# Kernel tuning notes

Hardware: AMD Instinct MI355X
Metric: run time of the kernel (lower is better)

Reference implementation:

```python
import jax, jax.numpy as jnp
import numpy as np

N_NODES = 50000
N_EDGES = 800000
IN_DIM = 128
HID = 128
N_GRAPHS = 64


def setup_inputs() -> dict:
    key = jax.random.key(0)
    ks = jax.random.split(key, 12)
    edge_index = jax.random.randint(ks[0], (2, N_EDGES), 0, N_NODES, dtype=jnp.int64)
    edge_weight = jax.random.uniform(ks[1], (N_EDGES,), dtype=jnp.float32)
    input_feature = jax.random.normal(ks[2], (N_NODES, IN_DIM), dtype=jnp.float32)
    graph_indicator = jnp.sort(jax.random.randint(ks[3], (N_NODES,), 0, N_GRAPHS, dtype=jnp.int64))
    s = 0.05
    W1 = jax.random.normal(ks[4], (IN_DIM, HID), dtype=jnp.float32) * s
    b1 = jnp.zeros((HID,), jnp.float32)
    W2 = jax.random.normal(ks[5], (HID, HID), dtype=jnp.float32) * s
    b2 = jnp.zeros((HID,), jnp.float32)
    W3 = jax.random.normal(ks[6], (HID, HID), dtype=jnp.float32) * s
    b3 = jnp.zeros((HID,), jnp.float32)
    wa = jax.random.normal(ks[7], (3 * HID, 1), dtype=jnp.float32) * s
    ba = jnp.zeros((1,), jnp.float32)
    Wf = jax.random.normal(ks[8], (3 * HID * 2, IN_DIM), dtype=jnp.float32) * s
    bf = jnp.zeros((IN_DIM,), jnp.float32)
    return dict(edge_index=edge_index, edge_weight=edge_weight,
                input_feature=input_feature, graph_indicator=graph_indicator,
                W1=W1, b1=b1, W2=W2, b2=b2, W3=W3, b3=b3,
                wa=wa, ba=ba, Wf=Wf, bf=bf)


def reference(edge_index, edge_weight, input_feature, graph_indicator,
              W1, b1, W2, b2, W3, b3, wa, ba, Wf, bf):
    src, dst = edge_index[0], edge_index[1]

    def gcn(x, W, b):
        # GraphConvolution: adj @ (x @ W) + b, adj given as weighted edge list
        support = x @ W  # [N, d_out]
        msg = edge_weight[:, None] * support[src]  # [E, d_out] gather
        return jax.ops.segment_sum(msg, dst, num_segments=N_NODES) + b

    g1 = jax.nn.relu(gcn(input_feature, W1, b1))
    g2 = jax.nn.relu(gcn(g1, W2, b2))
    g3 = jax.nn.relu(gcn(g2, W3, b3))
    h = jnp.concatenate([g1, g2, g3], axis=1)  # [N, 3*HID]

    # SelfAttentionPooling: attention score via a 1-dim GraphConvolution, tanh gate
    score = jnp.tanh(gcn(h, wa, ba))  # [N, 1]
    pool = h * score

    # segment avg / max pooling per graph
    seg_sum = jax.ops.segment_sum(pool, graph_indicator, num_segments=N_GRAPHS)
    counts = jax.ops.segment_sum(jnp.ones((N_NODES, 1), pool.dtype), graph_indicator,
                                 num_segments=N_GRAPHS)
    avg = seg_sum / jnp.maximum(counts, 1.0)
    mx = jax.ops.segment_max(pool, graph_indicator, num_segments=N_GRAPHS)
    pooled = jnp.concatenate([avg, mx], axis=1)  # [G, 6*HID]

    return jax.nn.relu(pooled @ Wf + bf)  # [G, IN_DIM]
```

## Files before the change

kernel.cpp:

```cpp
#include <hip/hip_runtime.h>
#include <math.h>

#define HID 128
#define POOL_SEG 16
#define WT_STRIDE 136
#define ELL_D 96
#define SC_CHUNK 2048

typedef __attribute__((ext_vector_type(8))) short short8;
typedef __attribute__((ext_vector_type(4))) float float4v;

__device__ inline short f2bf(float f) {
  unsigned u = __builtin_bit_cast(unsigned, f);
  unsigned r = (u + 0x7fff + ((u >> 16) & 1)) >> 16;
  return (short)r;
}
__device__ inline unsigned pack2bf(float lo, float hi) {
  return (unsigned)(unsigned short)f2bf(lo) | ((unsigned)(unsigned short)f2bf(hi) << 16);
}
__device__ inline float bflo(unsigned u) { return __builtin_bit_cast(float, u << 16); }
__device__ inline float bfhi(unsigned u) { return __builtin_bit_cast(float, u & 0xffff0000u); }
__device__ inline float bf2f(unsigned short s) { return __builtin_bit_cast(float, (unsigned)s << 16); }

__global__ void detect_flags(const int* __restrict__ ei, const int* __restrict__ gi,
                             int* __restrict__ flags, int n_nodes) {
  if (blockIdx.x == 0 && threadIdx.x == 0) {
    int nz = 0;
    for (int i = 1; i < 64; i += 2) nz |= ei[i];
    flags[0] = (nz == 0) ? 1 : 0;
    flags[1] = (gi[n_nodes - 1] == 0) ? 1 : 0;
  }
}

__global__ void scatter_ell(const void* __restrict__ ei_raw, const int* __restrict__ flags,
                            const float* __restrict__ ew, int* __restrict__ cursor,
                            int2* __restrict__ ell, int E, int N) {
  int group = blockIdx.x & 7;
  int chunk = blockIdx.x >> 3;
  int rng = (N + 7) / 8;
  int lo = group * rng;
  int hi = lo + rng; if (hi > N) hi = N;
  int base = chunk * SC_CHUNK;
  bool is64 = flags[0] != 0;
  const long long* p64 = (const long long*)ei_raw;
  const int* p32 = (const int*)ei_raw;
  for (int i = 0; i < SC_CHUNK; i += 256) {
    int e = base + i + threadIdx.x;
    if (e < E) {
      int d = is64 ? (int)p64[E + e] : p32[E + e];
      if (d >= lo && d < hi) {
        int s = is64 ? (int)p64[e] : p32[e];
        int r = atomicAdd(&cursor[d], 1);
        if (r < ELL_D)
          ell[(size_t)d * ELL_D + r] = make_int2(s, __builtin_bit_cast(int, ew[e]));
      }
    }
  }
}

__global__ void convert_w(const float* __restrict__ W1, const float* __restrict__ W2,
                          const float* __restrict__ W3, short* __restrict__ T1,
                          short* __restrict__ T2, short* __restrict__ T3) {
  int i = blockIdx.x * blockDim.x + threadIdx.x;
  int which = i >> 14, idx = i & 16383;
  int k = idx >> 7, n = idx & 127;
  const float* W = (which == 0) ? W1 : ((which == 1) ? W2 : W3);
  short* T = (which == 0) ? T1 : ((which == 1) ? T2 : T3);
  T[n * WT_STRIDE + k] = f2bf(W[idx]);
}

__global__ __launch_bounds__(256) void gemm_mfma(const float* __restrict__ Af,
                                                 const unsigned short* __restrict__ Abf,
                                                 const short* __restrict__ Wt,
                                                 unsigned short* __restrict__ C,
                                                 int n, int a_is_bf16) {
  __shared__ short Wlds[128 * WT_STRIDE];
  int t = threadIdx.x;
  {
    const ulonglong2* gsrc = (const ulonglong2*)Wt;
    ulonglong2* ldst = (ulonglong2*)Wlds;
    for (int i = t; i < (128 * WT_STRIDE) / 8; i += 256) ldst[i] = gsrc[i];
  }
  __syncthreads();

  int wave = t >> 6, lane = t & 63;
  int quad = lane >> 4, l15 = lane & 15;
  int m0 = blockIdx.x * 64 + wave * 16;

  int m = m0 + l15; if (m >= n) m = n - 1;
  short8 afrag[4];
  if (a_is_bf16) {
    const unsigned short* Arow = Abf + (size_t)m * 128;
#pragma unroll
    for (int c = 0; c < 4; c++) afrag[c] = *(const short8*)(Arow + c * 32 + quad * 8);
  } else {
    const float* Arow = Af + (size_t)m * 128;
#pragma unroll
    for (int c = 0; c < 4; c++) {
      int k0 = c * 32 + quad * 8;
      float4 x = *(const float4*)(Arow + k0);
      float4 y = *(const float4*)(Arow + k0 + 4);
      short8 a;
      a[0] = f2bf(x.x); a[1] = f2bf(x.y); a[2] = f2bf(x.z); a[3] = f2bf(x.w);
      a[4] = f2bf(y.x); a[5] = f2bf(y.y); a[6] = f2bf(y.z); a[7] = f2bf(y.w);
      afrag[c] = a;
    }
  }

  float4v acc[8];
#pragma unroll
  for (int tt = 0; tt < 8; tt++) acc[tt] = (float4v){0.f, 0.f, 0.f, 0.f};

#pragma unroll
  for (int c = 0; c < 4; c++) {
    int kb = c * 32 + quad * 8;
#pragma unroll
    for (int tt = 0; tt < 8; tt++) {
      const short8* bp = (const short8*)&Wlds[(tt * 16 + l15) * WT_STRIDE + kb];
      acc[tt] = __builtin_amdgcn_mfma_f32_16x16x32_bf16(afrag[c], *bp, acc[tt], 0, 0, 0);
    }
  }

  int rbase = m0 + quad * 4;
#pragma unroll
  for (int tt = 0; tt < 8; tt++) {
    int col = tt * 16 + l15;
#pragma unroll
    for (int r = 0; r < 4; r++) {
      int row = rbase + r;
      if (row < n) C[(size_t)row * 128 + col] = (unsigned short)f2bf(acc[tt][r]);
    }
  }
}

__global__ void aggregate(const unsigned short* __restrict__ support,
                          const int* __restrict__ deg_arr,
                          const int2* __restrict__ ell,
                          const float* __restrict__ bias, unsigned short* __restrict__ out,
                          const unsigned short* __restrict__ g1p,
                          const unsigned short* __restrict__ g2p,
                          const float* __restrict__ wa,
                          float* __restrict__ s_pre,
                          int n, int do_score) {
  int gid = blockIdx.x * blockDim.x + threadIdx.x;
  int node = gid >> 4, q = gid & 15;
  if (node >= n) return;
  int deg = deg_arr[node]; if (deg > ELL_D) deg = ELL_D;
  const int2* row = ell + (size_t)node * ELL_D;
  float acc[8];
#pragma unroll
  for (int j = 0; j < 8; j++) acc[j] = 0.f;
  const uint4* s4 = (const uint4*)support;

  int i = 0;
  for (; i + 3 < deg; i += 4) {
    int2 r0 = row[i], r1 = row[i + 1], r2 = row[i + 2], r3 = row[i + 3];
    float w0 = __builtin_bit_cast(float, r0.y), w1 = __builtin_bit_cast(float, r1.y);
    float w2 = __builtin_bit_cast(float, r2.y), w3 = __builtin_bit_cast(float, r3.y);
    uint4 v0 = s4[(size_t)r0.x * 16 + q];
    uint4 v1 = s4[(size_t)r1.x * 16 + q];
    uint4 v2 = s4[(size_t)r2.x * 16 + q];
    uint4 v3 = s4[(size_t)r3.x * 16 + q];
    acc[0] += w0 * bflo(v0.x); acc[1] += w0 * bfhi(v0.x);
    acc[2] += w0 * bflo(v0.y); acc[3] += w0 * bfhi(v0.y);
    acc[4] += w0 * bflo(v0.z); acc[5] += w0 * bfhi(v0.z);
    acc[6] += w0 * bflo(v0.w); acc[7] += w0 * bfhi(v0.w);
    acc[0] += w1 * bflo(v1.x); acc[1] += w1 * bfhi(v1.x);
    acc[2] += w1 * bflo(v1.y); acc[3] += w1 * bfhi(v1.y);
    acc[4] += w1 * bflo(v1.z); acc[5] += w1 * bfhi(v1.z);
    acc[6] += w1 * bflo(v1.w); acc[7] += w1 * bfhi(v1.w);
    acc[0] += w2 * bflo(v2.x); acc[1] += w2 * bfhi(v2.x);
    acc[2] += w2 * bflo(v2.y); acc[3] += w2 * bfhi(v2.y);
    acc[4] += w2 * bflo(v2.z); acc[5] += w2 * bfhi(v2.z);
    acc[6] += w2 * bflo(v2.w); acc[7] += w2 * bfhi(v2.w);
    acc[0] += w3 * bflo(v3.x); acc[1] += w3 * bfhi(v3.x);
    acc[2] += w3 * bflo(v3.y); acc[3] += w3 * bfhi(v3.y);
    acc[4] += w3 * bflo(v3.z); acc[5] += w3 * bfhi(v3.z);
    acc[6] += w3 * bflo(v3.w); acc[7] += w3 * bfhi(v3.w);
  }
  for (; i < deg; i++) {
    int2 r0 = row[i];
    float w0 = __builtin_bit_cast(float, r0.y);
    uint4 v0 = s4[(size_t)r0.x * 16 + q];
    acc[0] += w0 * bflo(v0.x); acc[1] += w0 * bfhi(v0.x);
    acc[2] += w0 * bflo(v0.y); acc[3] += w0 * bfhi(v0.y);
    acc[4] += w0 * bflo(v0.z); acc[5] += w0 * bfhi(v0.z);
    acc[6] += w0 * bflo(v0.w); acc[7] += w0 * bfhi(v0.w);
  }

  float4 b0 = ((const float4*)bias)[q * 2];
  float4 b1 = ((const float4*)bias)[q * 2 + 1];
  acc[0] = fmaxf(acc[0] + b0.x, 0.f); acc[1] = fmaxf(acc[1] + b0.y, 0.f);
  acc[2] = fmaxf(acc[2] + b0.z, 0.f); acc[3] = fmaxf(acc[3] + b0.w, 0.f);
  acc[4] = fmaxf(acc[4] + b1.x, 0.f); acc[5] = fmaxf(acc[5] + b1.y, 0.f);
  acc[6] = fmaxf(acc[6] + b1.z, 0.f); acc[7] = fmaxf(acc[7] + b1.w, 0.f);

  uint4 o;
  o.x = pack2bf(acc[0], acc[1]); o.y = pack2bf(acc[2], acc[3]);
  o.z = pack2bf(acc[4], acc[5]); o.w = pack2bf(acc[6], acc[7]);
  ((uint4*)out)[(size_t)node * 16 + q] = o;

  if (do_score) {
    int d0 = q * 8;
    uint4 u1 = ((const uint4*)g1p)[(size_t)node * 16 + q];
    uint4 u2 = ((const uint4*)g2p)[(size_t)node * 16 + q];
    const float* wa1 = wa + d0;
    const float* wa2 = wa + 128 + d0;
    const float* wa3 = wa + 256 + d0;
    float sc = bflo(u1.x) * wa1[0] + bfhi(u1.x) * wa1[1]
             + bflo(u1.y) * wa1[2] + bfhi(u1.y) * wa1[3]
             + bflo(u1.z) * wa1[4] + bfhi(u1.z) * wa1[5]
             + bflo(u1.w) * wa1[6] + bfhi(u1.w) * wa1[7]
             + bflo(u2.x) * wa2[0] + bfhi(u2.x) * wa2[1]
             + bflo(u2.y) * wa2[2] + bfhi(u2.y) * wa2[3]
             + bflo(u2.z) * wa2[4] + bfhi(u2.z) * wa2[5]
             + bflo(u2.w) * wa2[6] + bfhi(u2.w) * wa2[7];
#pragma unroll
    for (int j = 0; j < 8; j++) sc += acc[j] * wa3[j];
#pragma unroll
    for (int m = 1; m < 16; m <<= 1) sc += __shfl_xor(sc, m, 64);
    if (q == 0) s_pre[node] = sc;
  }
}

__global__ void att_aggregate(const float* __restrict__ s_pre, const int* __restrict__ deg_arr,
                              const int2* __restrict__ ell,
                              const float* __restrict__ ba, float* __restrict__ score, int n) {
  int node = blockIdx.x * blockDim.x + threadIdx.x;
  if (node >= n) return;
  int deg = deg_arr[node]; if (deg > ELL_D) deg = ELL_D;
  const int2* row = ell + (size_t)node * ELL_D;
  float acc = 0.f;
  for (int i = 0; i < deg; i++) {
    int2 r = row[i];
    acc += __builtin_bit_cast(float, r.y) * s_pre[r.x];
  }
  score[node] = tanhf(acc + ba[0]);
}

__global__ void graph_bounds(const void* __restrict__ gi_raw, const int* __restrict__ flags,
                             int* __restrict__ gstart, int n, int ngraphs) {
  int g = threadIdx.x;
  if (g > ngraphs) return;
  if (g == ngraphs) { gstart[g] = n; return; }
  bool is64 = flags[1] != 0;
  const long long* g64 = (const long long*)gi_raw;
  const int* g32 = (const int*)gi_raw;
  int lo = 0, hi = n;
  while (lo < hi) {
    int mid = (lo + hi) >> 1;
    long long v = is64 ? g64[mid] : (long long)g32[mid];
    if (v < (long long)g) lo = mid + 1; else hi = mid;
  }
  gstart[g] = lo;
}

__global__ __launch_bounds__(384) void pool_partial(const unsigned short* __restrict__ g1,
                                                    const unsigned short* __restrict__ g2,
                                                    const unsigned short* __restrict__ g3,
                                                    const float* __restrict__ score,
                                                    const int* __restrict__ gstart,
                                                    float* __restrict__ part) {
  int g = blockIdx.x / POOL_SEG, seg = blockIdx.x % POOL_SEG;
  int d = threadIdx.x;
  int sg = d >> 7, dd = d & 127;
  const unsigned short* gp = (sg == 0) ? g1 : ((sg == 1) ? g2 : g3);
  int s = gstart[g], e = gstart[g + 1];
  int len = e - s;
  int chunk = (len + POOL_SEG - 1) / POOL_SEG;
  int ns = s + seg * chunk;
  int ne = ns + chunk; if (ne > e) ne = e;
  float sum = 0.f, mx = -3.402823466e38f;
  for (int node = ns; node < ne; node++) {
    float sc = score[node];
    float v = bf2f(gp[(size_t)node * 128 + dd]) * sc;
    sum += v;
    mx = fmaxf(mx, v);
  }
  size_t base = (size_t)blockIdx.x * 768;
  part[base + d] = sum;
  part[base + 384 + d] = mx;
}

__global__ __launch_bounds__(384) void pool_combine(const float* __restrict__ part,
                                                    const int* __restrict__ gstart,
                                                    float* __restrict__ pooled) {
  int g = blockIdx.x;
  int d = threadIdx.x;
  float sum = 0.f, mx = -3.402823466e38f;
  for (int seg = 0; seg < POOL_SEG; seg++) {
    size_t base = ((size_t)g * POOL_SEG + seg) * 768;
    sum += part[base + d];
    mx = fmaxf(mx, part[base + 384 + d]);
  }
  float cnt = (float)(gstart[g + 1] - gstart[g]);
  pooled[(size_t)g * 768 + d] = sum / fmaxf(cnt, 1.0f);
  pooled[(size_t)g * 768 + 384 + d] = mx;
}

__global__ __launch_bounds__(128) void final_gemm(const float* __restrict__ pooled,
                                                  const float* __restrict__ Wf,
                                                  const float* __restrict__ bf,
                                                  float* __restrict__ out) {
  int g = blockIdx.x;
  int c = threadIdx.x;
  __shared__ float row[768];
  for (int i = c; i < 768; i += 128) row[i] = pooled[(size_t)g * 768 + i];
  __syncthreads();
  float acc = bf[c];
#pragma unroll 8
  for (int k = 0; k < 768; k++) acc += row[k] * Wf[k * 128 + c];
  out[(size_t)g * 128 + c] = fmaxf(acc, 0.f);
}

extern "C" void kernel_launch(void* const* d_in, const int* in_sizes, int n_in,
                              void* d_out, int out_size, void* d_ws, size_t ws_size,
                              hipStream_t stream) {
  const void* ei_raw = d_in[0];
  const float* ew    = (const float*)d_in[1];
  const float* X     = (const float*)d_in[2];
  const void* gi_raw = d_in[3];
  const float* W1 = (const float*)d_in[4];  const float* b1 = (const float*)d_in[5];
  const float* W2 = (const float*)d_in[6];  const float* b2 = (const float*)d_in[7];
  const float* W3 = (const float*)d_in[8];  const float* b3 = (const float*)d_in[9];
  const float* wa = (const float*)d_in[10]; const float* ba = (const float*)d_in[11];
  const float* Wf = (const float*)d_in[12]; const float* bf = (const float*)d_in[13];
  float* out = (float*)d_out;

  const int E = in_sizes[1];
  const int N = in_sizes[2] / 128;
  const int G = out_size / 128;

  char* ws = (char*)d_ws;
  size_t off = 0;
  auto take = [&](size_t bytes) {
    char* p = ws + off;
    off = (off + bytes + 255) & ~(size_t)255;
    return p;
  };
  int*   flags   = (int*)take(16);
  int*   cursor  = (int*)take((size_t)N * 4);
  int2*  ell     = (int2*)take((size_t)N * ELL_D * 8);
  short* wt1     = (short*)take((size_t)128 * WT_STRIDE * 2);
  short* wt2     = (short*)take((size_t)128 * WT_STRIDE * 2);
  short* wt3     = (short*)take((size_t)128 * WT_STRIDE * 2);
  unsigned short* support = (unsigned short*)take((size_t)N * 128 * 2);
  unsigned short* g1      = (unsigned short*)take((size_t)N * 128 * 2);
  unsigned short* g2      = (unsigned short*)take((size_t)N * 128 * 2);
  unsigned short* g3      = (unsigned short*)take((size_t)N * 128 * 2);
  float* s_pre   = (float*)take((size_t)N * 4);
  float* score   = (float*)take((size_t)N * 4);
  int*   gstart  = (int*)take((size_t)(G + 1) * 4);
  float* part    = (float*)take((size_t)G * POOL_SEG * 768 * 4);
  float* pooled  = (float*)take((size_t)G * 768 * 4);
  if (off > ws_size) return;

  hipMemsetAsync(cursor, 0, (size_t)N * 4, stream);
  detect_flags<<<1, 64, 0, stream>>>((const int*)ei_raw, (const int*)gi_raw, flags, N);
  convert_w<<<(3 * 16384 + 255) / 256, 256, 0, stream>>>(W1, W2, W3, wt1, wt2, wt3);
  {
    int chunks = (E + SC_CHUNK - 1) / SC_CHUNK;
    scatter_ell<<<8 * chunks, 256, 0, stream>>>(ei_raw, flags, ew, cursor, ell, E, N);
  }

  const int GB = (N + 63) / 64;
  const int AB = (N * 16 + 255) / 256;
  gemm_mfma<<<GB, 256, 0, stream>>>(X, (const unsigned short*)nullptr, wt1, support, N, 0);
  aggregate<<<AB, 256, 0, stream>>>(support, cursor, ell, b1, g1,
                                    nullptr, nullptr, nullptr, nullptr, N, 0);
  gemm_mfma<<<GB, 256, 0, stream>>>((const float*)nullptr, g1, wt2, support, N, 1);
  aggregate<<<AB, 256, 0, stream>>>(support, cursor, ell, b2, g2,
                                    nullptr, nullptr, nullptr, nullptr, N, 0);
  gemm_mfma<<<GB, 256, 0, stream>>>((const float*)nullptr, g2, wt3, support, N, 1);
  aggregate<<<AB, 256, 0, stream>>>(support, cursor, ell, b3, g3,
                                    g1, g2, wa, s_pre, N, 1);

  att_aggregate<<<(N + 255) / 256, 256, 0, stream>>>(s_pre, cursor, ell, ba, score, N);

  graph_bounds<<<1, 128, 0, stream>>>(gi_raw, flags, gstart, N, G);
  pool_partial<<<G * POOL_SEG, 384, 0, stream>>>(g1, g2, g3, score, gstart, part);
  pool_combine<<<G, 384, 0, stream>>>(part, gstart, pooled);
  final_gemm<<<G, 128, 0, stream>>>(pooled, Wf, bf, out);
}
```

Measured before the change: 350.1 us.

## Precompact edge arrays, shrink ELL width, use fixed-point integer accumulation

A new prep_edges pass converts the edge list once into a compact int32 destination array and a packed (src, weight) array. The eight scatter_ell range passes now read 4-byte destinations instead of possibly 64-bit indices, which cuts the scatter kernel's repeated global reads. ELL_D is halved from 96 to 48, shrinking the ELL buffer. Aggregations now accumulate in 16384-scaled integers, making sums independent of the atomic-driven edge order. The integer path adds a float-to-int conversion per term, and a node with more than 48 in-edges would silently lose edges.

Result: slower. 365.9 us (+4.5%).

```diff
diff --git a/kernel.cpp b/kernel.cpp
--- a/kernel.cpp
+++ b/kernel.cpp
@@ -4,8 +4,10 @@
 #define HID 128
 #define POOL_SEG 16
 #define WT_STRIDE 136
-#define ELL_D 96
+#define ELL_D 48
 #define SC_CHUNK 2048
+#define FXS 16384.0f
+#define FXI (1.0f/16384.0f)
 
 typedef __attribute__((ext_vector_type(8))) short short8;
 typedef __attribute__((ext_vector_type(4))) float float4v;
@@ -32,27 +34,40 @@
   }
 }
 
-__global__ void scatter_ell(const void* __restrict__ ei_raw, const int* __restrict__ flags,
-                            const float* __restrict__ ew, int* __restrict__ cursor,
-                            int2* __restrict__ ell, int E, int N) {
+__global__ void prep_edges(const void* __restrict__ ei_raw, const int* __restrict__ flags,
+                           const float* __restrict__ ew, int* __restrict__ dst32,
+                           int2* __restrict__ sw, int E) {
+  int e = blockIdx.x * blockDim.x + threadIdx.x;
+  if (e >= E) return;
+  int s, d;
+  if (flags[0]) {
+    const long long* p = (const long long*)ei_raw;
+    s = (int)p[e]; d = (int)p[E + e];
+  } else {
+    const int* p = (const int*)ei_raw;
+    s = p[e]; d = p[E + e];
+  }
+  dst32[e] = d;
+  sw[e] = make_int2(s, __builtin_bit_cast(int, ew[e]));
+}
+
+__global__ void scatter_ell(const int* __restrict__ dst32, const int2* __restrict__ sw,
+                            int* __restrict__ cursor, int2* __restrict__ ell, int E, int N) {
   int group = blockIdx.x & 7;
   int chunk = blockIdx.x >> 3;
   int rng = (N + 7) / 8;
   int lo = group * rng;
   int hi = lo + rng; if (hi > N) hi = N;
   int base = chunk * SC_CHUNK;
-  bool is64 = flags[0] != 0;
-  const long long* p64 = (const long long*)ei_raw;
-  const int* p32 = (const int*)ei_raw;
   for (int i = 0; i < SC_CHUNK; i += 256) {
     int e = base + i + threadIdx.x;
     if (e < E) {
-      int d = is64 ? (int)p64[E + e] : p32[E + e];
+      int d = dst32[e];
       if (d >= lo && d < hi) {
-        int s = is64 ? (int)p64[e] : p32[e];
-        int r = atomicAdd(&cursor[d], 1);
-        if (r < ELL_D)
-          ell[(size_t)d * ELL_D + r] = make_int2(s, __builtin_bit_cast(int, ew[e]));
+        int2 r = sw[e];
+        int pos = atomicAdd(&cursor[d], 1);
+        if (pos < ELL_D)
+          ell[(size_t)d * ELL_D + pos] = r;
       }
     }
   }
@@ -147,57 +162,63 @@
   if (node >= n) return;
   int deg = deg_arr[node]; if (deg > ELL_D) deg = ELL_D;
   const int2* row = ell + (size_t)node * ELL_D;
-  float acc[8];
-#pragma unroll
-  for (int j = 0; j < 8; j++) acc[j] = 0.f;
+  int acc[8];
+#pragma unroll
+  for (int j = 0; j < 8; j++) acc[j] = 0;
   const uint4* s4 = (const uint4*)support;
 
   int i = 0;
   for (; i + 3 < deg; i += 4) {
     int2 r0 = row[i], r1 = row[i + 1], r2 = row[i + 2], r3 = row[i + 3];
-    float w0 = __builtin_bit_cast(float, r0.y), w1 = __builtin_bit_cast(float, r1.y);
-    float w2 = __builtin_bit_cast(float, r2.y), w3 = __builtin_bit_cast(float, r3.y);
+    float w0 = __builtin_bit_cast(float, r0.y) * FXS;
+    float w1 = __builtin_bit_cast(float, r1.y) * FXS;
+    float w2 = __builtin_bit_cast(float, r2.y) * FXS;
+    float w3 = __builtin_bit_cast(float, r3.y) * FXS;
     uint4 v0 = s4[(size_t)r0.x * 16 + q];
     uint4 v1 = s4[(size_t)r1.x * 16 + q];
     uint4 v2 = s4[(size_t)r2.x * 16 + q];
     uint4 v3 = s4[(size_t)r3.x * 16 + q];
-    acc[0] += w0 * bflo(v0.x); acc[1] += w0 * bfhi(v0.x);
-    acc[2] += w0 * bflo(v0.y); acc[3] += w0 * bfhi(v0.y);
-    acc[4] += w0 * bflo(v0.z); acc[5] += w0 * bfhi(v0.z);
-    acc[6] += w0 * bflo(v0.w); acc[7] += w0 * bfhi(v0.w);
-    acc[0] += w1 * bflo(v1.x); acc[1] += w1 * bfhi(v1.x);
-    acc[2] += w1 * bflo(v1.y); acc[3] += w1 * bfhi(v1.y);
-    acc[4] += w1 * bflo(v1.z); acc[5] += w1 * bfhi(v1.z);
-    acc[6] += w1 * bflo(v1.w); acc[7] += w1 * bfhi(v1.w);
-    acc[0] += w2 * bflo(v2.x); acc[1] += w2 * bfhi(v2.x);
-    acc[2] += w2 * bflo(v2.y); acc[3] += w2 * bfhi(v2.y);
-    acc[4] += w2 * bflo(v2.z); acc[5] += w2 * bfhi(v2.z);
-    acc[6] += w2 * bflo(v2.w); acc[7] += w2 * bfhi(v2.w);
-    acc[0] += w3 * bflo(v3.x); acc[1] += w3 * bfhi(v3.x);
-    acc[2] += w3 * bflo(v3.y); acc[3] += w3 * bfhi(v3.y);
-    acc[4] += w3 * bflo(v3.z); acc[5] += w3 * bfhi(v3.z);
-    acc[6] += w3 * bflo(v3.w); acc[7] += w3 * bfhi(v3.w);
+    acc[0] += __float2int_rn(w0 * bflo(v0.x)); acc[1] += __float2int_rn(w0 * bfhi(v0.x));
+    acc[2] += __float2int_rn(w0 * bflo(v0.y)); acc[3] += __float2int_rn(w0 * bfhi(v0.y));
+    acc[4] += __float2int_rn(w0 * bflo(v0.z)); acc[5] += __float2int_rn(w0 * bfhi(v0.z));
+    acc[6] += __float2int_rn(w0 * bflo(v0.w)); acc[7] += __float2int_rn(w0 * bfhi(v0.w));
+    acc[0] += __float2int_rn(w1 * bflo(v1.x)); acc[1] += __float2int_rn(w1 * bfhi(v1.x));
+    acc[2] += __float2int_rn(w1 * bflo(v1.y)); acc[3] += __float2int_rn(w1 * bfhi(v1.y));
+    acc[4] += __float2int_rn(w1 * bflo(v1.z)); acc[5] += __float2int_rn(w1 * bfhi(v1.z));
+    acc[6] += __float2int_rn(w1 * bflo(v1.w)); acc[7] += __float2int_rn(w1 * bfhi(v1.w));
+    acc[0] += __float2int_rn(w2 * bflo(v2.x)); acc[1] += __float2int_rn(w2 * bfhi(v2.x));
+    acc[2] += __float2int_rn(w2 * bflo(v2.y)); acc[3] += __float2int_rn(w2 * bfhi(v2.y));
+    acc[4] += __float2int_rn(w2 * bflo(v2.z)); acc[5] += __float2int_rn(w2 * bfhi(v2.z));
+    acc[6] += __float2int_rn(w2 * bflo(v2.w)); acc[7] += __float2int_rn(w2 * bfhi(v2.w));
+    acc[0] += __float2int_rn(w3 * bflo(v3.x)); acc[1] += __float2int_rn(w3 * bfhi(v3.x));
+    acc[2] += __float2int_rn(w3 * bflo(v3.y)); acc[3] += __float2int_rn(w3 * bfhi(v3.y));
+    acc[4] += __float2int_rn(w3 * bflo(v3.z)); acc[5] += __float2int_rn(w3 * bfhi(v3.z));
+    acc[6] += __float2int_rn(w3 * bflo(v3.w)); acc[7] += __float2int_rn(w3 * bfhi(v3.w));
   }
   for (; i < deg; i++) {
     int2 r0 = row[i];
-    float w0 = __builtin_bit_cast(float, r0.y);
+    float w0 = __builtin_bit_cast(float, r0.y) * FXS;
     uint4 v0 = s4[(size_t)r0.x * 16 + q];
-    acc[0] += w0 * bflo(v0.x); acc[1] += w0 * bfhi(v0.x);
-    acc[2] += w0 * bflo(v0.y); acc[3] += w0 * bfhi(v0.y);
-    acc[4] += w0 * bflo(v0.z); acc[5] += w0 * bfhi(v0.z);
-    acc[6] += w0 * bflo(v0.w); acc[7] += w0 * bfhi(v0.w);
-  }
+    acc[0] += __float2int_rn(w0 * bflo(v0.x)); acc[1] += __float2int_rn(w0 * bfhi(v0.x));
+    acc[2] += __float2int_rn(w0 * bflo(v0.y)); acc[3] += __float2int_rn(w0 * bfhi(v0.y));
+    acc[4] += __float2int_rn(w0 * bflo(v0.z)); acc[5] += __float2int_rn(w0 * bfhi(v0.z));
+    acc[6] += __float2int_rn(w0 * bflo(v0.w)); acc[7] += __float2int_rn(w0 * bfhi(v0.w));
+  }
+
+  float f[8];
+#pragma unroll
+  for (int j = 0; j < 8; j++) f[j] = (float)acc[j] * FXI;
 
   float4 b0 = ((const float4*)bias)[q * 2];
   float4 b1 = ((const float4*)bias)[q * 2 + 1];
-  acc[0] = fmaxf(acc[0] + b0.x, 0.f); acc[1] = fmaxf(acc[1] + b0.y, 0.f);
-  acc[2] = fmaxf(acc[2] + b0.z, 0.f); acc[3] = fmaxf(acc[3] + b0.w, 0.f);
-  acc[4] = fmaxf(acc[4] + b1.x, 0.f); acc[5] = fmaxf(acc[5] + b1.y, 0.f);
-  acc[6] = fmaxf(acc[6] + b1.z, 0.f); acc[7] = fmaxf(acc[7] + b1.w, 0.f);
+  f[0] = fmaxf(f[0] + b0.x, 0.f); f[1] = fmaxf(f[1] + b0.y, 0.f);
+  f[2] = fmaxf(f[2] + b0.z, 0.f); f[3] = fmaxf(f[3] + b0.w, 0.f);
+  f[4] = fmaxf(f[4] + b1.x, 0.f); f[5] = fmaxf(f[5] + b1.y, 0.f);
+  f[6] = fmaxf(f[6] + b1.z, 0.f); f[7] = fmaxf(f[7] + b1.w, 0.f);
 
   uint4 o;
-  o.x = pack2bf(acc[0], acc[1]); o.y = pack2bf(acc[2], acc[3]);
-  o.z = pack2bf(acc[4], acc[5]); o.w = pack2bf(acc[6], acc[7]);
+  o.x = pack2bf(f[0], f[1]); o.y = pack2bf(f[2], f[3]);
+  o.z = pack2bf(f[4], f[5]); o.w = pack2bf(f[6], f[7]);
   ((uint4*)out)[(size_t)node * 16 + q] = o;
 
   if (do_score) {
@@ -216,7 +237,7 @@
              + bflo(u2.z) * wa2[4] + bfhi(u2.z) * wa2[5]
              + bflo(u2.w) * wa2[6] + bfhi(u2.w) * wa2[7];
 #pragma unroll
-    for (int j = 0; j < 8; j++) sc += acc[j] * wa3[j];
+    for (int j = 0; j < 8; j++) sc += f[j] * wa3[j];
 #pragma unroll
     for (int m = 1; m < 16; m <<= 1) sc += __shfl_xor(sc, m, 64);
     if (q == 0) s_pre[node] = sc;
@@ -230,12 +251,12 @@
   if (node >= n) return;
   int deg = deg_arr[node]; if (deg > ELL_D) deg = ELL_D;
   const int2* row = ell + (size_t)node * ELL_D;
-  float acc = 0.f;
+  int acc = 0;
   for (int i = 0; i < deg; i++) {
     int2 r = row[i];
-    acc += __builtin_bit_cast(float, r.y) * s_pre[r.x];
-  }
-  score[node] = tanhf(acc + ba[0]);
+    acc += __float2int_rn(__builtin_bit_cast(float, r.y) * FXS * s_pre[r.x]);
+  }
+  score[node] = tanhf((float)acc * FXI + ba[0]);
 }
 
 __global__ void graph_bounds(const void* __restrict__ gi_raw, const int* __restrict__ flags,
@@ -340,6 +361,8 @@
   };
   int*   flags   = (int*)take(16);
   int*   cursor  = (int*)take((size_t)N * 4);
+  int*   dst32   = (int*)take((size_t)E * 4);
+  int2*  sw      = (int2*)take((size_t)E * 8);
   int2*  ell     = (int2*)take((size_t)N * ELL_D * 8);
   short* wt1     = (short*)take((size_t)128 * WT_STRIDE * 2);
   short* wt2     = (short*)take((size_t)128 * WT_STRIDE * 2);
@@ -357,10 +380,11 @@
 
   hipMemsetAsync(cursor, 0, (size_t)N * 4, stream);
   detect_flags<<<1, 64, 0, stream>>>((const int*)ei_raw, (const int*)gi_raw, flags, N);
+  prep_edges<<<(E + 255) / 256, 256, 0, stream>>>(ei_raw, flags, ew, dst32, sw, E);
   convert_w<<<(3 * 16384 + 255) / 256, 256, 0, stream>>>(W1, W2, W3, wt1, wt2, wt3);
   {
     int chunks = (E + SC_CHUNK - 1) / SC_CHUNK;
-    scatter_ell<<<8 * chunks, 256, 0, stream>>>(ei_raw, flags, ew, cursor, ell, E, N);
+    scatter_ell<<<8 * chunks, 256, 0, stream>>>(dst32, sw, cursor, ell, E, N);
   }
 
   const int GB = (N + 63) / 64;
```
